# Optimization experiments

Measured on AMD Instinct MI355X. Metric: run time of the kernel, lower is better.

Reference implementation:

```python
import jax, jax.numpy as jnp
import numpy as np

# static sizes from init_kwargs / input_specs
B = 8            # batch elements
NH = 16384       # high_res_points per sample
NL = 2048        # low_res_points per sample
F_HR = 64
F_LR = 128


def setup_inputs() -> dict:
    key = jax.random.key(0)
    k1, k2, k3, k4 = jax.random.split(key, 4)
    x_hr = jax.random.normal(k1, (B * NH, F_HR), jnp.float32)
    pos_hr = jax.random.normal(k2, (B * NH, 3), jnp.float32)
    x_lr = jax.random.normal(k3, (B * NL, F_LR), jnp.float32)
    pos_lr = jax.random.normal(k4, (B * NL, 3), jnp.float32)
    # PyG-style contiguous batch assignment (sorted)
    batch_hr = jnp.repeat(jnp.arange(B, dtype=jnp.int32), NH)
    batch_lr = jnp.repeat(jnp.arange(B, dtype=jnp.int32), NL)
    return dict(x_hr=x_hr, pos_hr=pos_hr, batch_hr=batch_hr,
                x_lr=x_lr, pos_lr=pos_lr, batch_lr=batch_lr)


def _knn1_gather(p_h, p_l, f_l):
    # p_h: [nh,3], p_l: [nl,3], f_l: [nl,F]
    # squared euclidean distances [nh,nl] via (a-b)^2 expansion
    d2 = (jnp.sum(p_h * p_h, axis=-1, keepdims=True)
          - 2.0 * (p_h @ p_l.T)
          + jnp.sum(p_l * p_l, axis=-1)[None, :])
    idx = jnp.argmin(d2, axis=1)            # [nh] nearest low-res index
    return jnp.take(f_l, idx, axis=0)       # k=1 interpolation == pure gather


def reference(x_hr, pos_hr, batch_hr, x_lr, pos_lr, batch_lr):
    nB = x_hr.shape[0] // NH  # static
    out_x = jnp.concatenate([x_hr, pos_hr], axis=1)          # [B*NH, F_HR+3]
    lr_feat = jnp.concatenate([x_lr, pos_lr], axis=1)        # [B*NL, F_LR+3]

    # batch vectors are contiguous repeats -> reshape to [B, n, ...]
    ph = pos_hr.reshape(nB, NH, 3)
    pl = pos_lr.reshape(nB, NL, 3)
    fl = lr_feat.reshape(nB, NL, F_LR + 3)

    interp = jax.vmap(_knn1_gather)(ph, pl, fl)              # [B, NH, F_LR+3]
    interp = interp.reshape(nB * NH, F_LR + 3)

    out_x = jnp.concatenate([out_x, interp], axis=1)         # [B*NH, F_HR+3+F_LR+3]
    return (out_x, jnp.zeros((out_x.shape[0], 3), out_x.dtype), batch_hr)
```

## Files before the change

### kernel.cpp

```cpp
#include <hip/hip_runtime.h>

#define NB    8
#define NH    16384
#define NL    2048
#define F_HR  64
#define F_LR  128
#define OUT_COLS 198

__global__ __launch_bounds__(512, 4) void mixed_kernel(
    const float* __restrict__ pos_hr,
    const float* __restrict__ pos_lr,
    const float* __restrict__ x_hr,
    int* __restrict__ out_idx,
    float* __restrict__ out)
{
    __shared__ float4 cand[NL];
    __shared__ float  pval[8][256];
    __shared__ float  gminL[256];
    __shared__ int    winw[256];
    __shared__ short  plist[8][256];
    __shared__ float  phsx[256], phsy[256], phsz[256];

    if (blockIdx.x < 512) {
        const int b  = blockIdx.x >> 6;
        const int p0 = blockIdx.x << 8;
        const int w  = threadIdx.x >> 6;
        const int l  = threadIdx.x & 63;

        const float* pl = pos_lr + (size_t)b * NL * 3;
        for (int j = threadIdx.x; j < NL; j += 512) {
            float x = pl[j * 3 + 0];
            float y = pl[j * 3 + 1];
            float z = pl[j * 3 + 2];
            cand[j] = make_float4(x, y, z, 0.5f * ((x * x + y * y) + z * z));
        }

        float phx[4], phy[4], phz[4];
#pragma unroll
        for (int m = 0; m < 4; ++m) {
            const int pt = p0 + (m << 6) + l;
            phx[m] = pos_hr[pt * 3 + 0];
            phy[m] = pos_hr[pt * 3 + 1];
            phz[m] = pos_hr[pt * 3 + 2];
        }
        if (w == 0) {
#pragma unroll
            for (int m = 0; m < 4; ++m) {
                const int ptl = (m << 6) + l;
                phsx[ptl] = phx[m]; phsy[ptl] = phy[m]; phsz[ptl] = phz[m];
            }
        }
        __syncthreads();

        float best0[4], best1[4];
#pragma unroll
        for (int m = 0; m < 4; ++m) { best0[m] = 3.4e38f; best1[m] = 3.4e38f; }

        const int base = w << 8;
        for (int j = 0; j < 256; j += 2) {
            const float4 c0 = cand[base + j];
            const float4 c1 = cand[base + j + 1];
#pragma unroll
            for (int m = 0; m < 4; ++m) {
                float d0 = fmaf(-phz[m], c0.z, fmaf(-phy[m], c0.y, fmaf(-phx[m], c0.x, c0.w)));
                float d1 = fmaf(-phz[m], c1.z, fmaf(-phy[m], c1.y, fmaf(-phx[m], c1.x, c1.w)));
                best0[m] = fminf(best0[m], d0);
                best1[m] = fminf(best1[m], d1);
            }
        }
#pragma unroll
        for (int m = 0; m < 4; ++m)
            pval[w][(m << 6) + l] = fminf(best0[m], best1[m]);
        __syncthreads();

        if (threadIdx.x < 256) {
            const int t = threadIdx.x;
            float g = pval[0][t]; int ww = 0;
#pragma unroll
            for (int q = 1; q < 8; ++q) {
                const float qv = pval[q][t];
                if (qv < g) { g = qv; ww = q; }
            }
            gminL[t] = g; winw[t] = ww;
        }
        __syncthreads();

        int cnt = 0;
#pragma unroll
        for (int m = 0; m < 4; ++m) {
            const int pt = (m << 6) + l;
            const bool pred = (winw[pt] == w);
            const unsigned long long mask = __ballot(pred);
            const int pos = __popcll(mask & ((1ull << l) - 1ull));
            if (pred) plist[w][cnt + pos] = (short)pt;
            cnt += __popcll(mask);
        }

        for (int i = 0; i < cnt; ++i) {
            const int pt = plist[w][i];
            const float qx = phsx[pt], qy = phsy[pt], qz = phsz[pt];
            const float g  = gminL[pt];
            int loc = 4;
#pragma unroll
            for (int k = 3; k >= 0; --k) {
                const float4 c = cand[base + (l << 2) + k];
                const float d = fmaf(-qz, c.z, fmaf(-qy, c.y, fmaf(-qx, c.x, c.w)));
                if (d == g) loc = k;
            }
            const unsigned long long mk = __ballot(loc < 4);
            if (mk) {
                const int firstlane = __ffsll((unsigned long long)mk) - 1;
                const int locf = __shfl(loc, firstlane);
                if (l == 0)
                    out_idx[p0 + pt] = b * NL + base + (firstlane << 2) + locf;
            }
        }
    } else {
        const int cb = blockIdx.x - 512;
        const int r0 = cb << 9;

#pragma unroll 4
        for (int e = threadIdx.x; e < 512 * 67; e += 512) {
            const int rl  = e / 67;
            const int c   = e - rl * 67;
            const int row = r0 + rl;
            const float v = (c < F_HR) ? x_hr[(row << 6) + c]
                                       : pos_hr[row * 3 + (c - F_HR)];
            out[row * OUT_COLS + c] = v;
        }

        const int R0 = NB * NH * OUT_COLS;
        const int Z  = NB * NH * 3;
        const int z0 = cb << 11;
#pragma unroll
        for (int e = threadIdx.x; e < 2048; e += 512) {
            const int i = z0 + e;
            out[R0 + i] = (i < Z) ? 0.0f : (float)((i - Z) >> 14);
        }
    }
}

#define GRID_B   3072
#define NTHREADS (GRID_B * 256)
#define GCOLS    131
#define TOTAL_G  (NB * NH * GCOLS)
#define GROW_STEP 6003
#define GCOL_STEP 39
#define BATCH    11

__global__ __launch_bounds__(256) void assemble_kernel(
    const float* __restrict__ x_lr,
    const float* __restrict__ pos_lr,
    const int* __restrict__ idx,
    float* __restrict__ out)
{
    const int tid = blockIdx.x * blockDim.x + threadIdx.x;

    int row = tid / GCOLS;
    int col = tid - row * GCOLS;

    for (int b = 0; b < 2; ++b) {
        int   rs[BATCH], cs[BATCH], ls[BATCH];
        float vs[BATCH];

#pragma unroll
        for (int k = 0; k < BATCH; ++k) {
            const int rc = row < NB * NH ? row : NB * NH - 1;
            rs[k] = row;
            cs[k] = col;
            ls[k] = idx[rc];
            col += GCOL_STEP;
            const int carry = (col >= GCOLS) ? 1 : 0;
            col -= carry ? GCOLS : 0;
            row += GROW_STEP + carry;
        }

#pragma unroll
        for (int k = 0; k < BATCH; ++k) {
            const int c = cs[k];
            const float* a = (c < F_LR) ? x_lr   + ls[k] * F_LR + c
                                        : pos_lr + ls[k] * 3    + (c - F_LR);
            vs[k] = *a;
        }

#pragma unroll
        for (int k = 0; k < BATCH; ++k) {
            const int i = tid + (b * BATCH + k) * NTHREADS;
            if (b == 1 && k == BATCH - 1) {
                if (i < TOTAL_G) out[rs[k] * OUT_COLS + 67 + cs[k]] = vs[k];
            } else {
                out[rs[k] * OUT_COLS + 67 + cs[k]] = vs[k];
            }
        }
    }
}

extern "C" void kernel_launch(void* const* d_in, const int* in_sizes, int n_in,
                              void* d_out, int out_size, void* d_ws, size_t ws_size,
                              hipStream_t stream) {
    const float* x_hr   = (const float*)d_in[0];
    const float* pos_hr = (const float*)d_in[1];
    const float* x_lr   = (const float*)d_in[3];
    const float* pos_lr = (const float*)d_in[4];

    int* idx = (int*)d_ws;

    mixed_kernel<<<dim3(768), dim3(512), 0, stream>>>(
        pos_hr, pos_lr, x_hr, idx, (float*)d_out);
    assemble_kernel<<<dim3(GRID_B), dim3(256), 0, stream>>>(
        x_lr, pos_lr, idx, (float*)d_out);
}
```

Before: 67.48 us.

## Fuse nearest-neighbor gather into the kNN kernel via shared-memory indices

Keeps each block's argmin indices in shared memory and has the same block gather the 131 low-res feature columns into the output, so the separate assemble kernel is gone. This removes one launch, the global index round-trip and the dependency gap between the two kernels. In exchange the gather work is serialized behind the kNN phase within each block and confined to 512 blocks instead of a wide dedicated grid, which may cut memory-level parallelism.

```diff
diff --git a/kernel.cpp b/kernel.cpp
--- a/kernel.cpp
+++ b/kernel.cpp
@@ -7,11 +7,11 @@
 #define F_LR  128
 #define OUT_COLS 198
 
-__global__ __launch_bounds__(512, 4) void mixed_kernel(
+__global__ __launch_bounds__(512, 4) void fused_kernel(
     const float* __restrict__ pos_hr,
     const float* __restrict__ pos_lr,
     const float* __restrict__ x_hr,
-    int* __restrict__ out_idx,
+    const float* __restrict__ x_lr,
     float* __restrict__ out)
 {
     __shared__ float4 cand[NL];
@@ -20,6 +20,7 @@
     __shared__ int    winw[256];
     __shared__ short  plist[8][256];
     __shared__ float  phsx[256], phsy[256], phsz[256];
+    __shared__ int    s_idx[256];
 
     if (blockIdx.x < 512) {
         const int b  = blockIdx.x >> 6;
@@ -112,7 +113,39 @@
                 const int firstlane = __ffsll((unsigned long long)mk) - 1;
                 const int locf = __shfl(loc, firstlane);
                 if (l == 0)
-                    out_idx[p0 + pt] = b * NL + base + (firstlane << 2) + locf;
+                    s_idx[pt] = b * NL + base + (firstlane << 2) + locf;
+            }
+        }
+        __syncthreads();
+
+        {
+            const int tid = threadIdx.x;
+            int rl = tid / 131;
+            int c  = tid - rl * 131;
+            for (int t = 0; t < 11; ++t) {
+                int rs[6], cs[6], ls[6];
+                float vs[6];
+#pragma unroll
+                for (int k = 0; k < 6; ++k) {
+                    rs[k] = rl; cs[k] = c;
+                    ls[k] = s_idx[rl < 256 ? rl : 255];
+                    c += 119;
+                    const int carry = (c >= 131) ? 1 : 0;
+                    c -= carry ? 131 : 0;
+                    rl += 3 + carry;
+                }
+#pragma unroll
+                for (int k = 0; k < 6; ++k) {
+                    const int cc = cs[k];
+                    const float* a = (cc < F_LR) ? x_lr   + ls[k] * F_LR + cc
+                                                 : pos_lr + ls[k] * 3    + (cc - F_LR);
+                    vs[k] = *a;
+                }
+#pragma unroll
+                for (int k = 0; k < 6; ++k) {
+                    if (t == 10 && k == 5 && tid + 33280 >= 33536) continue;
+                    out[(size_t)(p0 + rs[k]) * OUT_COLS + 67 + cs[k]] = vs[k];
+                }
             }
         }
     } else {
@@ -140,61 +173,6 @@
     }
 }
 
-#define GRID_B   3072
-#define NTHREADS (GRID_B * 256)
-#define GCOLS    131
-#define TOTAL_G  (NB * NH * GCOLS)
-#define GROW_STEP 6003
-#define GCOL_STEP 39
-#define BATCH    11
-
-__global__ __launch_bounds__(256) void assemble_kernel(
-    const float* __restrict__ x_lr,
-    const float* __restrict__ pos_lr,
-    const int* __restrict__ idx,
-    float* __restrict__ out)
-{
-    const int tid = blockIdx.x * blockDim.x + threadIdx.x;
-
-    int row = tid / GCOLS;
-    int col = tid - row * GCOLS;
-
-    for (int b = 0; b < 2; ++b) {
-        int   rs[BATCH], cs[BATCH], ls[BATCH];
-        float vs[BATCH];
-
-#pragma unroll
-        for (int k = 0; k < BATCH; ++k) {
-            const int rc = row < NB * NH ? row : NB * NH - 1;
-            rs[k] = row;
-            cs[k] = col;
-            ls[k] = idx[rc];
-            col += GCOL_STEP;
-            const int carry = (col >= GCOLS) ? 1 : 0;
-            col -= carry ? GCOLS : 0;
-            row += GROW_STEP + carry;
-        }
-
-#pragma unroll
-        for (int k = 0; k < BATCH; ++k) {
-            const int c = cs[k];
-            const float* a = (c < F_LR) ? x_lr   + ls[k] * F_LR + c
-                                        : pos_lr + ls[k] * 3    + (c - F_LR);
-            vs[k] = *a;
-        }
-
-#pragma unroll
-        for (int k = 0; k < BATCH; ++k) {
-            const int i = tid + (b * BATCH + k) * NTHREADS;
-            if (b == 1 && k == BATCH - 1) {
-                if (i < TOTAL_G) out[rs[k] * OUT_COLS + 67 + cs[k]] = vs[k];
-            } else {
-                out[rs[k] * OUT_COLS + 67 + cs[k]] = vs[k];
-            }
-        }
-    }
-}
-
 extern "C" void kernel_launch(void* const* d_in, const int* in_sizes, int n_in,
                               void* d_out, int out_size, void* d_ws, size_t ws_size,
                               hipStream_t stream) {
@@ -203,10 +181,6 @@
     const float* x_lr   = (const float*)d_in[3];
     const float* pos_lr = (const float*)d_in[4];
 
-    int* idx = (int*)d_ws;
-
-    mixed_kernel<<<dim3(768), dim3(512), 0, stream>>>(
-        pos_hr, pos_lr, x_hr, idx, (float*)d_out);
-    assemble_kernel<<<dim3(GRID_B), dim3(256), 0, stream>>>(
-        x_lr, pos_lr, idx, (float*)d_out);
+    fused_kernel<<<dim3(768), dim3(512), 0, stream>>>(
+        pos_hr, pos_lr, x_hr, x_lr, (float*)d_out);
 }
```

Measured after the change: 54.79 us. 18.8% less time.
